# Kernel optimization log

Hardware: AMD Instinct MI355X
Metric: run time of the kernel (lower is better)

## Reference

```python
import jax, jax.numpy as jnp
import numpy as np

N = 50000      # nodes
E = 800000     # edges
D = 256        # embed_dim
H = 8          # num_heads
HD = D // H    # head_dim = 32
F = 4 * D      # feedforward_dim = 1024
SCALE = D ** -0.5  # note: module scales by embed_dim**-0.5, not head_dim
EPS = 1e-5


def setup_inputs() -> dict:
    key = jax.random.key(0)
    ks = jax.random.split(key, 10)
    x = jax.random.normal(ks[0], (N, D), dtype=jnp.float32)
    edge_indices = jax.random.randint(ks[1], (2, E), 0, N, dtype=jnp.int32)
    s = 0.02
    return {
        "x": x,
        "edge_indices": edge_indices,
        "w_qkv": jax.random.normal(ks[2], (D, 3 * D), dtype=jnp.float32) * s,
        "b_qkv": jnp.zeros((3 * D,), dtype=jnp.float32),
        "ln1_g": jnp.ones((D,), dtype=jnp.float32),
        "ln1_b": jnp.zeros((D,), dtype=jnp.float32),
        "ln2_g": jnp.ones((D,), dtype=jnp.float32),
        "ln2_b": jnp.zeros((D,), dtype=jnp.float32),
        "w1": jax.random.normal(ks[3], (D, F), dtype=jnp.float32) * s,
        "b1": jnp.zeros((F,), dtype=jnp.float32),
        "w2": jax.random.normal(ks[4], (F, D), dtype=jnp.float32) * s,
        "b2": jnp.zeros((D,), dtype=jnp.float32),
    }


def _layer_norm(x, g, b):
    m = jnp.mean(x, axis=-1, keepdims=True)
    v = jnp.mean((x - m) ** 2, axis=-1, keepdims=True)
    return (x - m) * jax.lax.rsqrt(v + EPS) * g + b


def _self_attention(x, edge_indices, w_qkv, b_qkv):
    qkv = (x @ w_qkv + b_qkv).reshape(N, H, 3 * HD)
    q, k, v = qkv[..., :HD], qkv[..., HD:2 * HD], qkv[..., 2 * HD:]
    rows, cols = edge_indices[0], edge_indices[1]
    # per-edge, per-head attention logits: [E, H]
    alpha = jnp.einsum('ehd,ehd->eh', q[rows], k[cols]) * SCALE
    # sparse softmax over each row (destination node) segment
    m = jax.ops.segment_max(alpha, rows, num_segments=N)       # [N, H]
    ea = jnp.exp(alpha - m[rows])                              # [E, H]
    denom = jax.ops.segment_sum(ea, rows, num_segments=N)      # [N, H]
    w = ea / denom[rows]                                       # [E, H]
    # per-head SpMM: out[r] += w_e * v[c]  -> [N, H, HD]
    out = jax.ops.segment_sum(w[:, :, None] * v[cols], rows, num_segments=N)
    return out.reshape(N, D)


def reference(x, edge_indices, w_qkv, b_qkv, ln1_g, ln1_b, ln2_g, ln2_b, w1, b1, w2, b2):
    # post-norm (norm_first=False), dropout=0
    x = _layer_norm(x + _self_attention(x, edge_indices, w_qkv, b_qkv), ln1_g, ln1_b)
    ffn = jax.nn.relu(x @ w1 + b1) @ w2 + b2
    x = _layer_norm(x + ffn, ln2_g, ln2_b)
    return x
```

## Files before the change

kernel.cpp:

```cpp
#include <hip/hip_runtime.h>
#include <hip/hip_bf16.h>

#define N_NODES 50000
#define E_EDGES 800000
#define D_MODEL 256
#define H_HEADS 8
#define HDIM    32
#define F_FFN   1024
#define ATT_SCALE 0.0625f
#define LN_EPS  1e-5f
#define NB_SCAN 196

typedef __attribute__((ext_vector_type(8))) short bf16x8;
typedef __attribute__((ext_vector_type(8))) unsigned short u16x8;
typedef __attribute__((ext_vector_type(4))) float f32x4;

__device__ __forceinline__ float bf2f(__hip_bfloat16 v) { return __bfloat162float(v); }
__device__ __forceinline__ __hip_bfloat16 f2bf(float v) { return __float2bfloat16(v); }
__device__ __forceinline__ unsigned short bfbits(float f) {
    __hip_bfloat16 h = __float2bfloat16(f);
    return *reinterpret_cast<unsigned short*>(&h);
}

__device__ __forceinline__ void unpack_bf8(uint4 u, float* f) {
    f[0] = __uint_as_float(u.x << 16); f[1] = __uint_as_float(u.x & 0xFFFF0000u);
    f[2] = __uint_as_float(u.y << 16); f[3] = __uint_as_float(u.y & 0xFFFF0000u);
    f[4] = __uint_as_float(u.z << 16); f[5] = __uint_as_float(u.z & 0xFFFF0000u);
    f[6] = __uint_as_float(u.w << 16); f[7] = __uint_as_float(u.w & 0xFFFF0000u);
}

template<int CTRL>
__device__ __forceinline__ float dpp_add(float v) {
    int t = __builtin_amdgcn_update_dpp(0, __float_as_int(v), CTRL, 0xF, 0xF, true);
    return v + __int_as_float(t);
}

__device__ __forceinline__ void load_lds16(const void* g, void* l) {
    __builtin_amdgcn_global_load_lds(
        (const __attribute__((address_space(1))) unsigned*)g,
        (__attribute__((address_space(3))) unsigned*)l, 16, 0, 0);
}

#define WAITV(N) asm volatile("s_waitcnt vmcnt(" #N ")" ::: "memory")
#define SBAR()   { __builtin_amdgcn_sched_barrier(0); __builtin_amdgcn_s_barrier(); \
                   __builtin_amdgcn_sched_barrier(0); }


#define PREP_X   3200000
#define PREP_WQ  (768 * 256)
#define PREP_W1  (1024 * 256)
#define PREP_W2  (256 * 1024)
#define PREP_BQ  768
#define PREP_B1  1024
#define PREP_TOT (PREP_X + PREP_WQ + PREP_W1 + PREP_W2 + PREP_BQ + PREP_B1 + N_NODES)
__global__ void prep_kernel(const float* __restrict__ x, unsigned short* __restrict__ xb,
                            const float* __restrict__ wq, __hip_bfloat16* __restrict__ wtq,
                            const float* __restrict__ w1, __hip_bfloat16* __restrict__ wt1,
                            const float* __restrict__ w2, __hip_bfloat16* __restrict__ wt2,
                            const float* __restrict__ bq, float* __restrict__ bqp,
                            const float* __restrict__ b1, float* __restrict__ b1p,
                            unsigned* __restrict__ counts, unsigned* __restrict__ cursor) {
    int i = blockIdx.x * blockDim.x + threadIdx.x;
    if (i < PREP_X) {
        float4 v = reinterpret_cast<const float4*>(x)[i];
        ushort4 o;
        o.x = bfbits(v.x); o.y = bfbits(v.y); o.z = bfbits(v.z); o.w = bfbits(v.w);
        reinterpret_cast<ushort4*>(xb)[i] = o;
        return;
    }
    i -= PREP_X;
    if (i < PREP_WQ) {
        int n = i >> 8, k = i & 255;
        int s = n >> 8, prel = n & 255;
        int d = (prel & 192) + ((prel & 15) << 2) + ((prel >> 4) & 3);
        int co = (d >> 5) * 96 + s * 32 + (d & 31);
        wtq[i] = f2bf(wq[(size_t)k * 768 + co]);
        return;
    }
    i -= PREP_WQ;
    if (i < PREP_W1) {
        int n = i >> 8, k = i & 255;
        int f = (n & ~63) + ((n & 15) << 2) + ((n >> 4) & 3);
        wt1[i] = f2bf(w1[(size_t)k * 1024 + f]);
        return;
    }
    i -= PREP_W1;
    if (i < PREP_W2) {
        int n = i >> 10, k = i & 1023;
        wt2[i] = f2bf(w2[(size_t)k * 256 + n]);
        return;
    }
    i -= PREP_W2;
    if (i < PREP_BQ) {
        int s = i >> 8, prel = i & 255;
        int d = (prel & 192) + ((prel & 15) << 2) + ((prel >> 4) & 3);
        bqp[i] = bq[(d >> 5) * 96 + s * 32 + (d & 31)];
        return;
    }
    i -= PREP_BQ;
    if (i < PREP_B1) {
        int f = (i & ~63) + ((i & 15) << 2) + ((i >> 4) & 3);
        b1p[i] = b1[f];
        return;
    }
    i -= PREP_B1;
    if (i < N_NODES) { counts[i] = 0u; cursor[i] = 0u; }
}

template<bool RELU, int EPI, int KT>
__global__ __launch_bounds__(256)
void mfma_gemm(const __hip_bfloat16* __restrict__ A,
               const __hip_bfloat16* __restrict__ Wt,
               const float* __restrict__ bias,
               __hip_bfloat16* __restrict__ outp,
               __hip_bfloat16* __restrict__ qb,
               unsigned char* __restrict__ kv8,
               int M, int Ncols) {
    __shared__ short Al[3][128 * 32];
    __shared__ short Bl[3][128 * 32];
    const int t = threadIdx.x;
    const int wave = t >> 6, lane = t & 63;

    unsigned flat = blockIdx.y * gridDim.x + blockIdx.x;
    unsigned nwg = gridDim.x * gridDim.y;
    unsigned q8 = nwg >> 3, r8 = nwg & 7;
    unsigned xcd = flat & 7, pos = flat >> 3;
    unsigned wg = (xcd < r8) ? (xcd * (q8 + 1) + pos)
                             : (r8 * (q8 + 1) + (xcd - r8) * q8 + pos);
    const int m0 = (int)(wg / gridDim.x) * 128;
    const int n0 = (int)(wg % gridDim.x) * 128;

    const int wr = wave >> 1, wc = wave & 1;

    const int srow = lane >> 2;
    const int skp  = (lane & 3) ^ ((lane >> 3) & 3);
    const int c0 = wave * 2;
    int ar0 = m0 + c0 * 16 + srow;      if (ar0 >= M) ar0 = M - 1;
    int ar1 = m0 + c0 * 16 + 16 + srow; if (ar1 >= M) ar1 = M - 1;
    const __hip_bfloat16* ga0 = A + (size_t)ar0 * KT + skp * 8;
    const __hip_bfloat16* ga1 = A + (size_t)ar1 * KT + skp * 8;
    const __hip_bfloat16* gb0 = Wt + (size_t)(n0 + c0 * 16 + srow) * KT + skp * 8;
    const __hip_bfloat16* gb1 = Wt + (size_t)(n0 + c0 * 16 + 16 + srow) * KT + skp * 8;

    const int lh = lane & 15, q = lane >> 4;
    const int qs = q ^ ((lane >> 1) & 3);
    const short* faB = &Al[0][(wr * 64 + lh) * 32 + qs * 8];
    const short* fbB = &Bl[0][(wc * 64 + lh) * 32 + qs * 8];

    f32x4 acc[4][4] = {};

#define GSTAGE(B)                                    \
    load_lds16(ga0, &Al[B][c0 * 512]);               \
    load_lds16(ga1, &Al[B][c0 * 512 + 512]);         \
    load_lds16(gb0, &Bl[B][c0 * 512]);               \
    load_lds16(gb1, &Bl[B][c0 * 512 + 512]);         \
    ga0 += 32; ga1 += 32; gb0 += 32; gb1 += 32;

#define GSTEP(FA, FB)                                                       \
    {                                                                       \
        bf16x8 af[4], bfr[4];                                               \
        _Pragma("unroll")                                                   \
        for (int i = 0; i < 4; i++) {                                       \
            af[i]  = *reinterpret_cast<const bf16x8*>((FA) + i * 16 * 32);  \
            bfr[i] = *reinterpret_cast<const bf16x8*>((FB) + i * 16 * 32);  \
        }                                                                   \
        _Pragma("unroll")                                                   \
        for (int mi = 0; mi < 4; mi++)                                      \
            _Pragma("unroll")                                               \
            for (int nj = 0; nj < 4; nj++)                                  \
                acc[mi][nj] = __builtin_amdgcn_mfma_f32_16x16x32_bf16(      \
                    af[mi], bfr[nj], acc[mi][nj], 0, 0, 0);                 \
    }

    constexpr int ns = KT >> 5;
    GSTAGE(0)
    GSTAGE(1)
#pragma unroll
    for (int s = 0; s < ns; ++s) {
        if (s < ns - 1) { WAITV(4); } else { WAITV(0); }
        SBAR();
        if (s + 2 < ns) {
            switch ((s + 2) % 3) {
                case 0: { GSTAGE(0) } break;
                case 1: { GSTAGE(1) } break;
                default: { GSTAGE(2) } break;
            }
        }
        const short* fa = faB + (s % 3) * 4096;
        const short* fb = fbB + (s % 3) * 4096;
        GSTEP(fa, fb)
    }
#undef GSTAGE
#undef GSTEP

    const int B = n0 + wc * 64;
    const int gnbase = B + lh;
    float bv[4];
#pragma unroll
    for (int nj = 0; nj < 4; nj++) bv[nj] = bias[gnbase + nj * 16];

    if (EPI == 0) {
        const int sec = B >> 8;
        const int c = ((B & 255) >> 6) * 16 + lh;
#pragma unroll
        for (int mi = 0; mi < 4; mi++) {
            int gmb = m0 + wr * 64 + mi * 16 + q * 4;
#pragma unroll
            for (int r = 0; r < 4; r++) {
                int gm = gmb + r;
                if (gm >= M) continue;
                float v0 = acc[mi][0][r] + bv[0];
                float v1 = acc[mi][1][r] + bv[1];
                float v2 = acc[mi][2][r] + bv[2];
                float v3 = acc[mi][3][r] + bv[3];
                if (sec == 0) {
                    ushort4 o;
                    o.x = bfbits(v0); o.y = bfbits(v1); o.z = bfbits(v2); o.w = bfbits(v3);
                    *reinterpret_cast<ushort4*>(qb + (size_t)gm * 256 + c * 4) = o;
                } else {
                    unsigned u = (unsigned)__builtin_amdgcn_cvt_pk_fp8_f32(v0, v1, 0, false);
                    u = (unsigned)__builtin_amdgcn_cvt_pk_fp8_f32(v2, v3, (int)u, true);
                    *reinterpret_cast<unsigned*>(
                        kv8 + (size_t)gm * 512 + c * 8 + (sec == 1 ? 0 : 4)) = u;
                }
            }
        }
    } else {
        const int cb = B + lh * 4;
#pragma unroll
        for (int mi = 0; mi < 4; mi++) {
            int gmb = m0 + wr * 64 + mi * 16 + q * 4;
#pragma unroll
            for (int r = 0; r < 4; r++) {
                int gm = gmb + r;
                if (gm >= M) continue;
                float v0 = acc[mi][0][r] + bv[0];
                float v1 = acc[mi][1][r] + bv[1];
                float v2 = acc[mi][2][r] + bv[2];
                float v3 = acc[mi][3][r] + bv[3];
                if (RELU) {
                    v0 = fmaxf(v0, 0.f); v1 = fmaxf(v1, 0.f);
                    v2 = fmaxf(v2, 0.f); v3 = fmaxf(v3, 0.f);
                }
                ushort4 o;
                o.x = bfbits(v0); o.y = bfbits(v1); o.z = bfbits(v2); o.w = bfbits(v3);
                *reinterpret_cast<ushort4*>(outp + (size_t)gm * Ncols + cb) = o;
            }
        }
    }
}

__global__ __launch_bounds__(512)
void ffn2_ln_kernel(const __hip_bfloat16* __restrict__ A,
                    const __hip_bfloat16* __restrict__ Wt,
                    const float* __restrict__ bias,
                    const __hip_bfloat16* __restrict__ resid,
                    const float* __restrict__ g, const float* __restrict__ bb,
                    float* __restrict__ out, int M) {
    __shared__ short LDS[3][(64 + 256) * 32];
    const int t = threadIdx.x;
    const int wave = t >> 6, lane = t & 63;
    const int m0 = blockIdx.x * 64;
    const int wr = wave >> 2, wc = wave & 3;

    const int srow = lane >> 2;
    const int skp  = (lane & 3) ^ ((lane >> 3) & 3);

    const __hip_bfloat16* gsrc0; int loff0;
    const __hip_bfloat16* gsrc1; int loff1;
    const __hip_bfloat16* gsrc2; int loff2;
    {
#define STAGE_INIT(GS, LO, C)                                            \
        if ((C) < 4) {                                                   \
            int r_ = m0 + (C) * 16 + srow; if (r_ >= M) r_ = M - 1;      \
            GS = A + (size_t)r_ * 1024 + skp * 8;                        \
            LO = (C) * 512;                                              \
        } else {                                                         \
            GS = Wt + (size_t)(((C) - 4) * 16 + srow) * 1024 + skp * 8;  \
            LO = 2048 + ((C) - 4) * 512;                                 \
        }
        STAGE_INIT(gsrc0, loff0, wave)
        STAGE_INIT(gsrc1, loff1, wave + 8)
        int c2 = (wave < 4) ? wave + 16 : 16;
        STAGE_INIT(gsrc2, loff2, c2)
#undef STAGE_INIT
    }

    const int lh = lane & 15, q = lane >> 4;
    const int qs = q ^ ((lane >> 1) & 3);
    const short* faB = &LDS[0][(wr * 32 + lh) * 32 + qs * 8];
    const short* fbB = &LDS[0][2048 + (wc * 64 + lh) * 32 + qs * 8];

    f32x4 acc[2][4] = {};

#define FFN2_STAGE(BUF)                                      \
    load_lds16(gsrc0, &LDS[BUF][loff0]);                     \
    load_lds16(gsrc1, &LDS[BUF][loff1]);                     \
    if (wave < 4) load_lds16(gsrc2, &LDS[BUF][loff2]);       \
    gsrc0 += 32; gsrc1 += 32; gsrc2 += 32;

#define FFN2_STEP(FA, FB)                                                   \
    {                                                                       \
        bf16x8 af[2], bfr[4];                                               \
        _Pragma("unroll")                                                   \
        for (int i = 0; i < 2; i++)                                         \
            af[i] = *reinterpret_cast<const bf16x8*>((FA) + i * 16 * 32);   \
        _Pragma("unroll")                                                   \
        for (int i = 0; i < 4; i++)                                         \
            bfr[i] = *reinterpret_cast<const bf16x8*>((FB) + i * 16 * 32);  \
        _Pragma("unroll")                                                   \
        for (int mi = 0; mi < 2; mi++)                                      \
            _Pragma("unroll")                                               \
            for (int nj = 0; nj < 4; nj++)                                  \
                acc[mi][nj] = __builtin_amdgcn_mfma_f32_16x16x32_bf16(      \
                    af[mi], bfr[nj], acc[mi][nj], 0, 0, 0);                 \
    }

    FFN2_STAGE(0)
    FFN2_STAGE(1)
#pragma unroll
    for (int s = 0; s < 32; ++s) {
        if (s < 31) {
            if (wave < 4) { WAITV(3); } else { WAITV(2); }
        } else {
            WAITV(0);
        }
        SBAR();
        if (s + 2 < 32) {
            switch ((s + 2) % 3) {
                case 0: { FFN2_STAGE(0) } break;
                case 1: { FFN2_STAGE(1) } break;
                default: { FFN2_STAGE(2) } break;
            }
        }
        const short* fa = faB + (s % 3) * 10240;
        const short* fb = fbB + (s % 3) * 10240;
        FFN2_STEP(fa, fb)
    }
    WAITV(0);
    SBAR();
#undef FFN2_STAGE
#undef FFN2_STEP

    const int colbase = wc * 64 + lh;
    float bv[4], gv[4], bbv[4];
#pragma unroll
    for (int nj = 0; nj < 4; nj++) {
        bv[nj]  = bias[colbase + nj * 16];
        gv[nj]  = g[colbase + nj * 16];
        bbv[nj] = bb[colbase + nj * 16];
    }

    float ps[2][4], pq[2][4];
#pragma unroll
    for (int mi = 0; mi < 2; mi++) {
#pragma unroll
        for (int r = 0; r < 4; r++) {
            int gm = m0 + wr * 32 + mi * 16 + q * 4 + r;
            int rgm = (gm < M) ? gm : M - 1;
            float s = 0.f, s2 = 0.f;
#pragma unroll
            for (int nj = 0; nj < 4; nj++) {
                float v = acc[mi][nj][r] + bv[nj]
                        + bf2f(resid[(size_t)rgm * 256 + colbase + nj * 16]);
                acc[mi][nj][r] = v;
                s += v; s2 += v * v;
            }
            ps[mi][r] = s; pq[mi][r] = s2;
        }
    }
#pragma unroll
    for (int off = 1; off <= 8; off <<= 1) {
#pragma unroll
        for (int mi = 0; mi < 2; mi++)
#pragma unroll
            for (int r = 0; r < 4; r++) {
                ps[mi][r] += __shfl_xor(ps[mi][r], off);
                pq[mi][r] += __shfl_xor(pq[mi][r], off);
            }
    }
    float* rs = (float*)(&LDS[0][0]);
    float* rq = rs + 256;
    if (lh == 0) {
#pragma unroll
        for (int mi = 0; mi < 2; mi++)
#pragma unroll
            for (int r = 0; r < 4; r++) {
                int m = wr * 32 + mi * 16 + q * 4 + r;
                rs[m * 4 + wc] = ps[mi][r];
                rq[m * 4 + wc] = pq[mi][r];
            }
    }
    __syncthreads();

#pragma unroll
    for (int mi = 0; mi < 2; mi++) {
#pragma unroll
        for (int r = 0; r < 4; r++) {
            int m = wr * 32 + mi * 16 + q * 4 + r;
            int gm = m0 + m;
            if (gm >= M) continue;
            float4 rsv = *reinterpret_cast<const float4*>(&rs[m * 4]);
            float4 rqv = *reinterpret_cast<const float4*>(&rq[m * 4]);
            float S  = (rsv.x + rsv.y) + (rsv.z + rsv.w);
            float S2 = (rqv.x + rqv.y) + (rqv.z + rqv.w);
            float mean = S * (1.f / (float)D_MODEL);
            float var  = S2 * (1.f / (float)D_MODEL) - mean * mean;
            float inv  = rsqrtf(var + LN_EPS);
#pragma unroll
            for (int nj = 0; nj < 4; nj++)
                out[(size_t)gm * 256 + colbase + nj * 16] =
                    (acc[mi][nj][r] - mean) * inv * gv[nj] + bbv[nj];
        }
    }
}

__global__ void count_kernel(const int* __restrict__ rows, unsigned* __restrict__ counts) {
    int e = blockIdx.x * blockDim.x + threadIdx.x;
    if (e < E_EDGES) atomicAdd(&counts[rows[e]], 1u);
}

__global__ void scan_blk_kernel(const unsigned* __restrict__ counts,
                                unsigned* __restrict__ offs, unsigned* __restrict__ bsum) {
    __shared__ unsigned sh[256];
    int t = threadIdx.x;
    int i = blockIdx.x * 256 + t;
    unsigned v = (i < N_NODES) ? counts[i] : 0u;
    sh[t] = v;
    __syncthreads();
#pragma unroll
    for (int off = 1; off < 256; off <<= 1) {
        unsigned u = (t >= off) ? sh[t - off] : 0u;
        __syncthreads();
        sh[t] += u;
        __syncthreads();
    }
    if (i < N_NODES) offs[i] = sh[t] - v;
    if (t == 255) bsum[blockIdx.x] = sh[255];
}

__global__ void scan_top_kernel(const unsigned* __restrict__ bsum, unsigned* __restrict__ bpre) {
    __shared__ unsigned sh[256];
    int t = threadIdx.x;
    unsigned v = (t < NB_SCAN) ? bsum[t] : 0u;
    sh[t] = v;
    __syncthreads();
#pragma unroll
    for (int off = 1; off < 256; off <<= 1) {
        unsigned u = (t >= off) ? sh[t - off] : 0u;
        __syncthreads();
        sh[t] += u;
        __syncthreads();
    }
    if (t < NB_SCAN) bpre[t] = sh[t] - v;
    if (t == NB_SCAN - 1) bpre[NB_SCAN] = sh[t];
}

__global__ void scatter_kernel(const int* __restrict__ rows, const int* __restrict__ cols,
                               const unsigned* __restrict__ offsets,
                               const unsigned* __restrict__ bpre,
                               unsigned* __restrict__ cursor,
                               int* __restrict__ scol) {
    int e = blockIdx.x * blockDim.x + threadIdx.x;
    if (e >= E_EDGES) return;
    int r = rows[e];
    unsigned idx = atomicAdd(&cursor[r], 1u);
    scol[offsets[r] + bpre[r >> 8] + idx] = cols[e];
}

__global__ __launch_bounds__(128)
void att_agg_kernel(const __hip_bfloat16* __restrict__ qb,
                    const unsigned char* __restrict__ kv8,
                    const unsigned* __restrict__ offsets,
                    const unsigned* __restrict__ bpre,
                    const int* __restrict__ scol,
                    const __hip_bfloat16* __restrict__ xres,
                    const float* __restrict__ g, const float* __restrict__ bb,
                    __hip_bfloat16* __restrict__ xn) {
    int n = blockIdx.x * 2 + (threadIdx.x >> 6);
    if (n >= N_NODES) return;
    const int lam = threadIdx.x & 63;
    const int hl  = lam & 31;
    const int sel = lam >> 5;
    const unsigned hlb = hl * 16;
    unsigned beg = offsets[n] + bpre[n >> 8];
    unsigned end = (n + 1 == N_NODES) ? bpre[NB_SCAN]
                                      : offsets[n + 1] + bpre[(n + 1) >> 8];

    float qv[8];
    {
        uint4 u = *reinterpret_cast<const uint4*>(qb + (size_t)n * 256 + hl * 8);
        unpack_bf8(u, qv);
#pragma unroll
        for (int i = 0; i < 8; i++) qv[i] *= ATT_SCALE;
    }

    float acc[8] = {};
    float l = 0.f;

#define PAIR_BODY(W, VMUL)                                                      \
    {                                                                           \
        auto k01 = __builtin_amdgcn_cvt_pk_f32_fp8((int)(W).x, false);          \
        auto k23 = __builtin_amdgcn_cvt_pk_f32_fp8((int)(W).x, true);           \
        auto k45 = __builtin_amdgcn_cvt_pk_f32_fp8((int)(W).z, false);          \
        auto k67 = __builtin_amdgcn_cvt_pk_f32_fp8((int)(W).z, true);           \
        float sv = qv[0] * k01[0] + qv[1] * k01[1] + qv[2] * k23[0]             \
                 + qv[3] * k23[1] + qv[4] * k45[0] + qv[5] * k45[1]             \
                 + qv[6] * k67[0] + qv[7] * k67[1];                             \
        sv = dpp_add<0xB1>(sv);                           \
        sv = dpp_add<0x4E>(sv);                           \
        float pv = __expf(sv) * (VMUL);                                         \
        l += pv;                                                                \
        auto v01 = __builtin_amdgcn_cvt_pk_f32_fp8((int)(W).y, false);          \
        auto v23 = __builtin_amdgcn_cvt_pk_f32_fp8((int)(W).y, true);           \
        auto v45 = __builtin_amdgcn_cvt_pk_f32_fp8((int)(W).w, false);          \
        auto v67 = __builtin_amdgcn_cvt_pk_f32_fp8((int)(W).w, true);           \
        acc[0] += pv * v01[0]; acc[1] += pv * v01[1];                           \
        acc[2] += pv * v23[0]; acc[3] += pv * v23[1];                           \
        acc[4] += pv * v45[0]; acc[5] += pv * v45[1];                           \
        acc[6] += pv * v67[0]; acc[7] += pv * v67[1];                           \
    }

    unsigned e = beg;
    unsigned oA = 0, oB = 0, oC = 0, oD = 0;
    if (e + 8 <= end) {
        oA = ((unsigned)scol[e + sel])     << 9;
        oB = ((unsigned)scol[e + 2 + sel]) << 9;
        oC = ((unsigned)scol[e + 4 + sel]) << 9;
        oD = ((unsigned)scol[e + 6 + sel]) << 9;
    }
    while (e + 8 <= end) {
        uint4 wa = *reinterpret_cast<const uint4*>(kv8 + (oA + hlb));
        uint4 wb = *reinterpret_cast<const uint4*>(kv8 + (oB + hlb));
        uint4 wc = *reinterpret_cast<const uint4*>(kv8 + (oC + hlb));
        uint4 wd = *reinterpret_cast<const uint4*>(kv8 + (oD + hlb));
        e += 8;
        if (e + 8 <= end) {
            oA = ((unsigned)scol[e + sel])     << 9;
            oB = ((unsigned)scol[e + 2 + sel]) << 9;
            oC = ((unsigned)scol[e + 4 + sel]) << 9;
            oD = ((unsigned)scol[e + 6 + sel]) << 9;
        }
        PAIR_BODY(wa, 1.0f)
        PAIR_BODY(wb, 1.0f)
        PAIR_BODY(wc, 1.0f)
        PAIR_BODY(wd, 1.0f)
    }
    for (; e + 2 <= end; e += 2) {
        unsigned o0 = ((unsigned)scol[e + sel]) << 9;
        uint4 wa = *reinterpret_cast<const uint4*>(kv8 + (o0 + hlb));
        PAIR_BODY(wa, 1.0f)
    }
    if (e < end) {
        unsigned o0 = ((unsigned)scol[e]) << 9;
        uint4 wa = *reinterpret_cast<const uint4*>(kv8 + (o0 + hlb));
        PAIR_BODY(wa, sel ? 0.0f : 1.0f)
    }
#undef PAIR_BODY

    l += __shfl_xor(l, 32);
#pragma unroll
    for (int i = 0; i < 8; i++) acc[i] += __shfl_xor(acc[i], 32);

    float inv_l = (l > 0.f) ? 1.f / l : 0.f;

    float tv[8];
    {
        float xv[8];
        uint4 u = *reinterpret_cast<const uint4*>(xres + (size_t)n * D_MODEL + hl * 8);
        unpack_bf8(u, xv);
#pragma unroll
        for (int i = 0; i < 8; i++) tv[i] = acc[i] * inv_l + xv[i];
    }

    float s = 0.f, s2 = 0.f;
#pragma unroll
    for (int i = 0; i < 8; i++) { s += tv[i]; s2 += tv[i] * tv[i]; }
#pragma unroll
    for (int off = 1; off <= 16; off <<= 1) {
        s  += __shfl_xor(s, off);
        s2 += __shfl_xor(s2, off);
    }
    float mean = s * (1.f / (float)D_MODEL);
    float var  = s2 * (1.f / (float)D_MODEL) - mean * mean;
    float inv  = rsqrtf(var + LN_EPS);

    if (sel == 0) {
        const float4* gp = reinterpret_cast<const float4*>(g);
        const float4* bp = reinterpret_cast<const float4*>(bb);
        float4 g0 = gp[hl * 2], g1 = gp[hl * 2 + 1];
        float4 b0 = bp[hl * 2], b1 = bp[hl * 2 + 1];
        float gv[8] = {g0.x, g0.y, g0.z, g0.w, g1.x, g1.y, g1.z, g1.w};
        float bv[8] = {b0.x, b0.y, b0.z, b0.w, b1.x, b1.y, b1.z, b1.w};
        u16x8 o;
#pragma unroll
        for (int i = 0; i < 8; i++)
            o[i] = bfbits((tv[i] - mean) * inv * gv[i] + bv[i]);
        *reinterpret_cast<u16x8*>(xn + (size_t)n * D_MODEL + hl * 8) = o;
    }
}

extern "C" void kernel_launch(void* const* d_in, const int* in_sizes, int n_in,
                              void* d_out, int out_size, void* d_ws, size_t ws_size,
                              hipStream_t stream) {
    const float* x     = (const float*)d_in[0];
    const int*   ei    = (const int*)d_in[1];
    const float* w_qkv = (const float*)d_in[2];
    const float* b_qkv = (const float*)d_in[3];
    const float* ln1_g = (const float*)d_in[4];
    const float* ln1_b = (const float*)d_in[5];
    const float* ln2_g = (const float*)d_in[6];
    const float* ln2_b = (const float*)d_in[7];
    const float* w1    = (const float*)d_in[8];
    const float* b1    = (const float*)d_in[9];
    const float* w2    = (const float*)d_in[10];
    const float* b2    = (const float*)d_in[11];
    const int* rows = ei;
    const int* cols = ei + E_EDGES;

    char* ws = (char*)d_ws;
    __hip_bfloat16* qb      = (__hip_bfloat16*)(ws + 0);
    unsigned char*  kv8     = (unsigned char*)(ws + 25600000);
    __hip_bfloat16* hbuf    = (__hip_bfloat16*)(ws + 0);
    __hip_bfloat16* xb      = (__hip_bfloat16*)(ws + 102400000);
    __hip_bfloat16* wtq     = (__hip_bfloat16*)(ws + 128000000);
    __hip_bfloat16* wt1     = (__hip_bfloat16*)(ws + 128400000);
    __hip_bfloat16* wt2     = (__hip_bfloat16*)(ws + 129000000);
    unsigned*       counts  = (unsigned*)(ws + 129600000);
    unsigned*       offsets = (unsigned*)(ws + 129800000);
    unsigned*       cursor  = (unsigned*)(ws + 130000008);
    int*            scol    = (int*)(ws + 130200008);
    unsigned*       bsum    = (unsigned*)(ws + 133400008);
    unsigned*       bpre    = (unsigned*)(ws + 133401032);
    float*          bqp     = (float*)(ws + 133500000);
    float*          b1p     = (float*)(ws + 133510000);
    __hip_bfloat16* xn      = (__hip_bfloat16*)(ws + 153600000);

    const int nbM = (N_NODES + 127) / 128;

    prep_kernel<<<(PREP_TOT + 255) / 256, 256, 0, stream>>>(
        x, (unsigned short*)xb, w_qkv, wtq, w1, wt1, w2, wt2,
        b_qkv, bqp, b1, b1p, counts, cursor);

    mfma_gemm<false, 0, 256><<<dim3(768 / 128, nbM), 256, 0, stream>>>(
        xb, wtq, bqp, nullptr, qb, kv8, N_NODES, 768);

    count_kernel<<<(E_EDGES + 255) / 256, 256, 0, stream>>>(rows, counts);
    scan_blk_kernel<<<NB_SCAN, 256, 0, stream>>>(counts, offsets, bsum);
    scan_top_kernel<<<1, 256, 0, stream>>>(bsum, bpre);
    scatter_kernel<<<(E_EDGES + 255) / 256, 256, 0, stream>>>(rows, cols, offsets, bpre,
                                                              cursor, scol);

    att_agg_kernel<<<(N_NODES + 1) / 2, 128, 0, stream>>>(qb, kv8, offsets, bpre, scol,
                                                          xb, ln1_g, ln1_b, xn);

    mfma_gemm<true, 1, 256><<<dim3(F_FFN / 128, nbM), 256, 0, stream>>>(
        xn, wt1, b1p, hbuf, nullptr, nullptr, N_NODES, F_FFN);

    ffn2_ln_kernel<<<(N_NODES + 63) / 64, 512, 0, stream>>>(hbuf, wt2, b2, xn, ln2_g, ln2_b,
                                                            (float*)d_out, N_NODES);
}
```

Before: 409.2 us.

## Fuse edge counting into prep kernel and double-buffer FFN2 staging

The per-edge row count atomics move into the prep kernel, so the separate count kernel launch goes away, and the counts and cursor arrays are now zeroed with memset calls instead of inside prep. Separately, the FFN2+LayerNorm kernel drops its three-buffer LDS pipeline with explicit vmcnt waits and uses a simpler two-buffer loop synchronised by __syncthreads. The double-buffer change lowers LDS use, which may allow more resident blocks, but it adds full barriers and a shallower prefetch depth. The memsets add two small operations in place of the one kernel launch removed.

```diff
diff --git a/kernel.cpp b/kernel.cpp
--- a/kernel.cpp
+++ b/kernel.cpp
@@ -46,21 +46,27 @@
                    __builtin_amdgcn_sched_barrier(0); }
 
 
+#define PREP_E   E_EDGES
 #define PREP_X   3200000
 #define PREP_WQ  (768 * 256)
 #define PREP_W1  (1024 * 256)
 #define PREP_W2  (256 * 1024)
 #define PREP_BQ  768
 #define PREP_B1  1024
-#define PREP_TOT (PREP_X + PREP_WQ + PREP_W1 + PREP_W2 + PREP_BQ + PREP_B1 + N_NODES)
-__global__ void prep_kernel(const float* __restrict__ x, unsigned short* __restrict__ xb,
+#define PREP_TOT (PREP_E + PREP_X + PREP_WQ + PREP_W1 + PREP_W2 + PREP_BQ + PREP_B1)
+__global__ void prep_kernel(const int* __restrict__ rows, unsigned* __restrict__ counts,
+                            const float* __restrict__ x, unsigned short* __restrict__ xb,
                             const float* __restrict__ wq, __hip_bfloat16* __restrict__ wtq,
                             const float* __restrict__ w1, __hip_bfloat16* __restrict__ wt1,
                             const float* __restrict__ w2, __hip_bfloat16* __restrict__ wt2,
                             const float* __restrict__ bq, float* __restrict__ bqp,
-                            const float* __restrict__ b1, float* __restrict__ b1p,
-                            unsigned* __restrict__ counts, unsigned* __restrict__ cursor) {
+                            const float* __restrict__ b1, float* __restrict__ b1p) {
     int i = blockIdx.x * blockDim.x + threadIdx.x;
+    if (i < PREP_E) {
+        atomicAdd(&counts[rows[i]], 1u);
+        return;
+    }
+    i -= PREP_E;
     if (i < PREP_X) {
         float4 v = reinterpret_cast<const float4*>(x)[i];
         ushort4 o;
@@ -103,8 +109,6 @@
         b1p[i] = b1[f];
         return;
     }
-    i -= PREP_B1;
-    if (i < N_NODES) { counts[i] = 0u; cursor[i] = 0u; }
 }
 
 template<bool RELU, int EPI, int KT>
@@ -257,7 +261,7 @@
                     const __hip_bfloat16* __restrict__ resid,
                     const float* __restrict__ g, const float* __restrict__ bb,
                     float* __restrict__ out, int M) {
-    __shared__ short LDS[3][(64 + 256) * 32];
+    __shared__ short LDS[2][(64 + 256) * 32];
     const int t = threadIdx.x;
     const int wave = t >> 6, lane = t & 63;
     const int m0 = blockIdx.x * 64;
@@ -288,8 +292,10 @@
 
     const int lh = lane & 15, q = lane >> 4;
     const int qs = q ^ ((lane >> 1) & 3);
-    const short* faB = &LDS[0][(wr * 32 + lh) * 32 + qs * 8];
-    const short* fbB = &LDS[0][2048 + (wc * 64 + lh) * 32 + qs * 8];
+    const short* fa0 = &LDS[0][(wr * 32 + lh) * 32 + qs * 8];
+    const short* fb0 = &LDS[0][2048 + (wc * 64 + lh) * 32 + qs * 8];
+    const short* fa1 = &LDS[1][(wr * 32 + lh) * 32 + qs * 8];
+    const short* fb1 = &LDS[1][2048 + (wc * 64 + lh) * 32 + qs * 8];
 
     f32x4 acc[2][4] = {};
 
@@ -317,28 +323,16 @@
     }
 
     FFN2_STAGE(0)
-    FFN2_STAGE(1)
-#pragma unroll
-    for (int s = 0; s < 32; ++s) {
-        if (s < 31) {
-            if (wave < 4) { WAITV(3); } else { WAITV(2); }
-        } else {
-            WAITV(0);
-        }
-        SBAR();
-        if (s + 2 < 32) {
-            switch ((s + 2) % 3) {
-                case 0: { FFN2_STAGE(0) } break;
-                case 1: { FFN2_STAGE(1) } break;
-                default: { FFN2_STAGE(2) } break;
-            }
-        }
-        const short* fa = faB + (s % 3) * 10240;
-        const short* fb = fbB + (s % 3) * 10240;
-        FFN2_STEP(fa, fb)
-    }
-    WAITV(0);
-    SBAR();
+    __syncthreads();
+
+    for (int s = 0; s < 32; s += 2) {
+        FFN2_STAGE(1)
+        FFN2_STEP(fa0, fb0)
+        __syncthreads();
+        if (s < 30) { FFN2_STAGE(0) }
+        FFN2_STEP(fa1, fb1)
+        __syncthreads();
+    }
 #undef FFN2_STAGE
 #undef FFN2_STEP
 
@@ -413,11 +407,6 @@
                     (acc[mi][nj][r] - mean) * inv * gv[nj] + bbv[nj];
         }
     }
-}
-
-__global__ void count_kernel(const int* __restrict__ rows, unsigned* __restrict__ counts) {
-    int e = blockIdx.x * blockDim.x + threadIdx.x;
-    if (e < E_EDGES) atomicAdd(&counts[rows[e]], 1u);
 }
 
 __global__ void scan_blk_kernel(const unsigned* __restrict__ counts,
@@ -507,8 +496,8 @@
         float sv = qv[0] * k01[0] + qv[1] * k01[1] + qv[2] * k23[0]             \
                  + qv[3] * k23[1] + qv[4] * k45[0] + qv[5] * k45[1]             \
                  + qv[6] * k67[0] + qv[7] * k67[1];                             \
-        sv = dpp_add<0xB1>(sv);                           \
-        sv = dpp_add<0x4E>(sv);                           \
+        sv = dpp_add<0xB1>(sv);                                                 \
+        sv = dpp_add<0x4E>(sv);                                                 \
         float pv = __expf(sv) * (VMUL);                                         \
         l += pv;                                                                \
         auto v01 = __builtin_amdgcn_cvt_pk_f32_fp8((int)(W).y, false);          \
@@ -638,14 +627,16 @@
 
     const int nbM = (N_NODES + 127) / 128;
 
+    hipMemsetAsync(counts, 0, N_NODES * sizeof(unsigned), stream);
+    hipMemsetAsync(cursor, 0, N_NODES * sizeof(unsigned), stream);
+
     prep_kernel<<<(PREP_TOT + 255) / 256, 256, 0, stream>>>(
-        x, (unsigned short*)xb, w_qkv, wtq, w1, wt1, w2, wt2,
-        b_qkv, bqp, b1, b1p, counts, cursor);
+        rows, counts, x, (unsigned short*)xb, w_qkv, wtq, w1, wt1, w2, wt2,
+        b_qkv, bqp, b1, b1p);
 
     mfma_gemm<false, 0, 256><<<dim3(768 / 128, nbM), 256, 0, stream>>>(
         xb, wtq, bqp, nullptr, qb, kv8, N_NODES, 768);
 
-    count_kernel<<<(E_EDGES + 255) / 256, 256, 0, stream>>>(rows, counts);
     scan_blk_kernel<<<NB_SCAN, 256, 0, stream>>>(counts, offsets, bsum);
     scan_top_kernel<<<1, 256, 0, stream>>>(bsum, bpre);
     scatter_kernel<<<(E_EDGES + 255) / 256, 256, 0, stream>>>(rows, cols, offsets, bpre,
```

Measured after the change: 414.9 us. Within noise of the previous version (+1.4%).
